# Kernel tuning notes

Hardware: AMD Instinct MI355X
Metric: run time of the kernel (lower is better)

Reference implementation:

```python
import jax, jax.numpy as jnp
import numpy as np

N_VIEWS = 8


def _trilinear(vol, pts):
    """Trilinear interpolation of vol [Nx,Ny,Nz] at pts [...,3] (voxel coords), zero outside."""
    nx, ny, nz = vol.shape
    x, y, z = pts[..., 0], pts[..., 1], pts[..., 2]
    x0f, y0f, z0f = jnp.floor(x), jnp.floor(y), jnp.floor(z)
    fx, fy, fz = x - x0f, y - y0f, z - z0f
    x0 = x0f.astype(jnp.int32)
    y0 = y0f.astype(jnp.int32)
    z0 = z0f.astype(jnp.int32)
    out = jnp.zeros(x.shape, vol.dtype)
    for dx in (0, 1):
        wx = fx if dx else (1.0 - fx)
        ix = x0 + dx
        vx = (ix >= 0) & (ix < nx)
        ixc = jnp.clip(ix, 0, nx - 1)
        for dy in (0, 1):
            wy = fy if dy else (1.0 - fy)
            iy = y0 + dy
            vxy = vx & (iy >= 0) & (iy < ny)
            iyc = jnp.clip(iy, 0, ny - 1)
            for dz in (0, 1):
                wz = fz if dz else (1.0 - fz)
                iz = z0 + dz
                valid = vxy & (iz >= 0) & (iz < nz)
                izc = jnp.clip(iz, 0, nz - 1)
                v = vol[ixc, iyc, izc]  # irregular gather
                out = out + jnp.where(valid, v, jnp.zeros((), vol.dtype)) * (wx * wy * wz)
    return out


def cone_project(vol, src_pos, det_center, det_u_vec, det_v_vec,
                 det_u, det_v, du, dv, voxel_spacing, n_steps):
    """Cone-beam forward projection: ray-march src->detector pixel, trilinear sampling."""
    nx, ny, nz = vol.shape
    us = (jnp.arange(det_u, dtype=vol.dtype) - (det_u - 1) / 2.0) * du
    vs = (jnp.arange(det_v, dtype=vol.dtype) - (det_v - 1) / 2.0) * dv
    # detector pixel world positions: [V, U, W, 3]
    det_pts = (det_center[:, None, None, :]
               + us[None, :, None, None] * det_u_vec[:, None, None, :]
               + vs[None, None, :, None] * det_v_vec[:, None, None, :])
    src = src_pos[:, None, None, :]            # [V,1,1,3]
    diff = det_pts - src                        # [V,U,W,3]
    ray_len = jnp.sqrt(jnp.sum(diff * diff, axis=-1))  # [V,U,W]
    step_len = ray_len / n_steps
    center = (jnp.array([nx, ny, nz], dtype=vol.dtype) - 1.0) / 2.0
    fracs = (jnp.arange(n_steps, dtype=vol.dtype) + 0.5) / n_steps

    def body(acc, s):
        p = src + s * diff                      # world coords [V,U,W,3]
        vox = p / voxel_spacing + center        # voxel coords
        return acc + _trilinear(vol, vox), None

    acc, _ = jax.lax.scan(body, jnp.zeros(ray_len.shape, vol.dtype), fracs)
    return acc * step_len


def setup_inputs() -> dict:
    key = jax.random.key(0)
    k1, k2 = jax.random.split(key)
    vol_shape = (256, 256, 256)
    x = 0.1 * jax.random.normal(k1, vol_shape, dtype=jnp.float32)
    reco = 0.1 * jax.random.normal(k2, vol_shape, dtype=jnp.float32)
    # circular cone-beam trajectory (units = voxels, spacing 1.0)
    sad, sdd = 400.0, 800.0  # source-axis / source-detector distance
    angles = np.linspace(0.0, np.pi, N_VIEWS, endpoint=False)
    ca, sa = np.cos(angles), np.sin(angles)
    zeros = np.zeros(N_VIEWS)
    src_pos = np.stack([-sad * ca, -sad * sa, zeros], axis=-1)
    det_center = np.stack([(sdd - sad) * ca, (sdd - sad) * sa, zeros], axis=-1)
    det_u_vec = np.stack([-sa, ca, zeros], axis=-1)
    det_v_vec = np.tile(np.array([0.0, 0.0, 1.0]), (N_VIEWS, 1))
    return {
        "x": x,
        "reco": reco,
        "src_pos": jnp.asarray(src_pos, jnp.float32),
        "det_center": jnp.asarray(det_center, jnp.float32),
        "det_u_vec": jnp.asarray(det_u_vec, jnp.float32),
        "det_v_vec": jnp.asarray(det_v_vec, jnp.float32),
        "du": 3.0,
        "dv": 3.0,
        "voxel_spacing": 1.0,
        "det_u": 128,
        "det_v": 128,
        "n_steps": 192,
    }


def reference(x, reco, src_pos, det_center, det_u_vec, det_v_vec,
              du, dv, voxel_spacing, det_u, det_v, n_steps):
    updated = x + reco
    sino = cone_project(updated, src_pos, det_center, det_u_vec, det_v_vec,
                        det_u, det_v, du, dv, voxel_spacing, n_steps)
    return sino, jax.nn.relu(updated)
```

## Files before the change

kernel.cpp:

```cpp
#include <hip/hip_runtime.h>
#include <math.h>

__global__ __launch_bounds__(256) void add_relu_kernel(
    const float* __restrict__ x,
    const float* __restrict__ reco,
    float* __restrict__ relu_out,
    float* __restrict__ upd_out,
    int n4)
{
    int i = blockIdx.x * blockDim.x + threadIdx.x;
    int stride = gridDim.x * blockDim.x;
    const float4* x4 = (const float4*)x;
    const float4* r4 = (const float4*)reco;
    float4* ro4 = (float4*)relu_out;
    float4* uo4 = (float4*)upd_out;
    for (; i < n4; i += stride) {
        float4 a = x4[i];
        float4 b = r4[i];
        float4 u;
        u.x = a.x + b.x;
        u.y = a.y + b.y;
        u.z = a.z + b.z;
        u.w = a.w + b.w;
        if (uo4) uo4[i] = u;
        float4 r;
        r.x = fmaxf(u.x, 0.0f);
        r.y = fmaxf(u.y, 0.0f);
        r.z = fmaxf(u.z, 0.0f);
        r.w = fmaxf(u.w, 0.0f);
        ro4[i] = r;
    }
}

template <int TWO>
__device__ __forceinline__ float fetch_corner(
    const float* __restrict__ vol_a,
    const float* __restrict__ vol_b,
    int ix, int iy, int iz,
    int nx, int ny, int nz)
{
    bool valid = (ix >= 0) & (ix < nx) & (iy >= 0) & (iy < ny) &
                 (iz >= 0) & (iz < nz);
    if (!valid) return 0.0f;
    int idx = (ix * ny + iy) * nz + iz;
    float v = vol_a[idx];
    if (TWO) v += vol_b[idx];
    return v;
}

__device__ __forceinline__ void clip_axis(float a, float b, float lo, float hi,
                                          float& t_lo, float& t_hi)
{
    if (fabsf(b) > 1e-6f) {
        float t0 = (lo - a) / b;
        float t1 = (hi - a) / b;
        float tmn = fminf(t0, t1);
        float tmx = fmaxf(t0, t1);
        t_lo = fmaxf(t_lo, tmn);
        t_hi = fminf(t_hi, tmx);
    } else {
        if (a <= lo || a >= hi) { t_lo = 1.0f; t_hi = 0.0f; }
    }
}

template <int TWO>
__global__ __launch_bounds__(256) void cone_project_seg_kernel(
    const float* __restrict__ vol_a,
    const float* __restrict__ vol_b,
    const float* __restrict__ src_pos,
    const float* __restrict__ det_center,
    const float* __restrict__ det_u_vec,
    const float* __restrict__ det_v_vec,
    const float* __restrict__ du_p,
    const float* __restrict__ dv_p,
    const float* __restrict__ spacing_p,
    const int* __restrict__ det_u_p,
    const int* __restrict__ det_v_p,
    const int* __restrict__ nsteps_p,
    float* __restrict__ sino,
    int n_views, int nx, int ny, int nz)
{
    const int det_u = *det_u_p;
    const int det_v = *det_v_p;
    const int n_steps = *nsteps_p;
    const float du = *du_p;
    const float dv = *dv_p;
    const float inv_sp = 1.0f / *spacing_p;

    const long total = (long)n_views * det_u * det_v;
    const int pix = threadIdx.x & 63;
    const int seg = threadIdx.x >> 6;
    const long idx = (long)blockIdx.x * 64 + pix;
    const bool live = idx < total;

    const long cidx = live ? idx : 0;
    const int v = (int)(cidx % det_v);
    const int u = (int)((cidx / det_v) % det_u);
    const int view = (int)(cidx / ((long)det_u * det_v));

    const float us = ((float)u - (det_u - 1) * 0.5f) * du;
    const float vs = ((float)v - (det_v - 1) * 0.5f) * dv;

    const float sx = src_pos[view * 3 + 0];
    const float sy = src_pos[view * 3 + 1];
    const float sz = src_pos[view * 3 + 2];

    const float dpx = det_center[view * 3 + 0] + us * det_u_vec[view * 3 + 0] + vs * det_v_vec[view * 3 + 0];
    const float dpy = det_center[view * 3 + 1] + us * det_u_vec[view * 3 + 1] + vs * det_v_vec[view * 3 + 1];
    const float dpz = det_center[view * 3 + 2] + us * det_u_vec[view * 3 + 2] + vs * det_v_vec[view * 3 + 2];

    const float dx = dpx - sx;
    const float dy = dpy - sy;
    const float dz = dpz - sz;
    const float ray_len = sqrtf(dx * dx + dy * dy + dz * dz);
    const float step_len = ray_len / (float)n_steps;

    const float cx = (nx - 1) * 0.5f;
    const float cy = (ny - 1) * 0.5f;
    const float cz = (nz - 1) * 0.5f;

    float t_lo = 0.0f, t_hi = 1.0f;
    clip_axis(sx * inv_sp + cx, dx * inv_sp, -1.0f, (float)nx, t_lo, t_hi);
    clip_axis(sy * inv_sp + cy, dy * inv_sp, -1.0f, (float)ny, t_lo, t_hi);
    clip_axis(sz * inv_sp + cz, dz * inv_sp, -1.0f, (float)nz, t_lo, t_hi);

    int i_min = 0, i_max = -1;
    if (t_hi > t_lo) {
        i_min = (int)floorf(t_lo * (float)n_steps - 0.5f) - 1;
        i_max = (int)ceilf(t_hi * (float)n_steps - 0.5f) + 1;
        i_min = max(i_min, 0);
        i_max = min(i_max, n_steps - 1);
    }
    if (!live) { i_min = 0; i_max = -1; }

    const int count = i_max - i_min + 1;
    const int per = (count + 3) >> 2;
    const int is = i_min + seg * per;
    const int ie = min(is + per - 1, i_max);

    const float inv_n = 1.0f / (float)n_steps;

    float acc = 0.0f;
    for (int i = is; i <= ie; ++i) {
        const float s = ((float)i + 0.5f) * inv_n;
        const float px = fmaf(s, dx, sx) * inv_sp + cx;
        const float py = fmaf(s, dy, sy) * inv_sp + cy;
        const float pz = fmaf(s, dz, sz) * inv_sp + cz;

        const float x0f = floorf(px);
        const float y0f = floorf(py);
        const float z0f = floorf(pz);
        const float fx = px - x0f;
        const float fy = py - y0f;
        const float fz = pz - z0f;
        const int x0 = (int)x0f;
        const int y0 = (int)y0f;
        const int z0 = (int)z0f;

        const float gx = 1.0f - fx;
        const float gy = 1.0f - fy;
        const float gz = 1.0f - fz;

        float samp = 0.0f;
        samp = fmaf(gx * gy * gz, fetch_corner<TWO>(vol_a, vol_b, x0,     y0,     z0,     nx, ny, nz), samp);
        samp = fmaf(gx * gy * fz, fetch_corner<TWO>(vol_a, vol_b, x0,     y0,     z0 + 1, nx, ny, nz), samp);
        samp = fmaf(gx * fy * gz, fetch_corner<TWO>(vol_a, vol_b, x0,     y0 + 1, z0,     nx, ny, nz), samp);
        samp = fmaf(gx * fy * fz, fetch_corner<TWO>(vol_a, vol_b, x0,     y0 + 1, z0 + 1, nx, ny, nz), samp);
        samp = fmaf(fx * gy * gz, fetch_corner<TWO>(vol_a, vol_b, x0 + 1, y0,     z0,     nx, ny, nz), samp);
        samp = fmaf(fx * gy * fz, fetch_corner<TWO>(vol_a, vol_b, x0 + 1, y0,     z0 + 1, nx, ny, nz), samp);
        samp = fmaf(fx * fy * gz, fetch_corner<TWO>(vol_a, vol_b, x0 + 1, y0 + 1, z0,     nx, ny, nz), samp);
        samp = fmaf(fx * fy * fz, fetch_corner<TWO>(vol_a, vol_b, x0 + 1, y0 + 1, z0 + 1, nx, ny, nz), samp);
        acc += samp;
    }

    __shared__ float red[256];
    red[threadIdx.x] = acc;
    __syncthreads();
    if (seg == 0 && live) {
        float tot = red[pix] + red[pix + 64] + red[pix + 128] + red[pix + 192];
        sino[idx] = tot * step_len;
    }
}

extern "C" void kernel_launch(void* const* d_in, const int* in_sizes, int n_in,
                              void* d_out, int out_size, void* d_ws, size_t ws_size,
                              hipStream_t stream) {
    const float* x          = (const float*)d_in[0];
    const float* reco       = (const float*)d_in[1];
    const float* src_pos    = (const float*)d_in[2];
    const float* det_center = (const float*)d_in[3];
    const float* det_u_vec  = (const float*)d_in[4];
    const float* det_v_vec  = (const float*)d_in[5];
    const float* du_p       = (const float*)d_in[6];
    const float* dv_p       = (const float*)d_in[7];
    const float* spacing_p  = (const float*)d_in[8];
    const int*   det_u_p    = (const int*)d_in[9];
    const int*   det_v_p    = (const int*)d_in[10];
    const int*   nsteps_p   = (const int*)d_in[11];

    const int n_vol = in_sizes[0];
    const int n_views = in_sizes[2] / 3;

    int n = 1;
    while ((long)(n + 1) * (n + 1) * (n + 1) <= (long)n_vol) ++n;
    const int nx = n, ny = n, nz = n;

    const int sino_size = out_size - n_vol;
    float* sino     = (float*)d_out;
    float* relu_out = (float*)d_out + sino_size;

    const bool use_ws = ws_size >= (size_t)n_vol * sizeof(float);
    float* upd = (float*)d_ws;

    const int n4 = n_vol / 4;
    add_relu_kernel<<<2048, 256, 0, stream>>>(
        x, reco, relu_out, use_ws ? upd : nullptr, n4);

    const int blocks = (sino_size + 63) / 64;
    if (use_ws) {
        cone_project_seg_kernel<0><<<blocks, 256, 0, stream>>>(
            upd, nullptr,
            src_pos, det_center, det_u_vec, det_v_vec,
            du_p, dv_p, spacing_p, det_u_p, det_v_p, nsteps_p,
            sino, n_views, nx, ny, nz);
    } else {
        cone_project_seg_kernel<1><<<blocks, 256, 0, stream>>>(
            x, reco,
            src_pos, det_center, det_u_vec, det_v_vec,
            du_p, dv_p, spacing_p, det_u_p, det_v_p, nsteps_p,
            sino, n_views, nx, ny, nz);
    }
}
```

Baseline: 238.1 us.

## Fuse add-relu and projection into one kernel with interleaved blocks

Merges the elementwise add+relu and the cone-beam projection into a single launch, spreading elementwise blocks evenly among projection blocks. The projector now reads x and reco directly and sums them per corner instead of reading a precomputed workspace volume. An interior fast path skips per-corner bounds checks. Each pixel's ray is split into eight segments instead of four. The trade is one launch and no workspace round-trip, paid for with twice the gather traffic per sample.

```diff
diff --git a/kernel.cpp b/kernel.cpp
--- a/kernel.cpp
+++ b/kernel.cpp
@@ -1,39 +1,10 @@
 #include <hip/hip_runtime.h>
 #include <math.h>
 
-__global__ __launch_bounds__(256) void add_relu_kernel(
-    const float* __restrict__ x,
-    const float* __restrict__ reco,
-    float* __restrict__ relu_out,
-    float* __restrict__ upd_out,
-    int n4)
-{
-    int i = blockIdx.x * blockDim.x + threadIdx.x;
-    int stride = gridDim.x * blockDim.x;
-    const float4* x4 = (const float4*)x;
-    const float4* r4 = (const float4*)reco;
-    float4* ro4 = (float4*)relu_out;
-    float4* uo4 = (float4*)upd_out;
-    for (; i < n4; i += stride) {
-        float4 a = x4[i];
-        float4 b = r4[i];
-        float4 u;
-        u.x = a.x + b.x;
-        u.y = a.y + b.y;
-        u.z = a.z + b.z;
-        u.w = a.w + b.w;
-        if (uo4) uo4[i] = u;
-        float4 r;
-        r.x = fmaxf(u.x, 0.0f);
-        r.y = fmaxf(u.y, 0.0f);
-        r.z = fmaxf(u.z, 0.0f);
-        r.w = fmaxf(u.w, 0.0f);
-        ro4[i] = r;
-    }
-}
-
-template <int TWO>
-__device__ __forceinline__ float fetch_corner(
+typedef float nfloat4 __attribute__((ext_vector_type(4)));
+
+
+__device__ __forceinline__ float fetch_corner2(
     const float* __restrict__ vol_a,
     const float* __restrict__ vol_b,
     int ix, int iy, int iz,
@@ -43,9 +14,7 @@
                  (iz >= 0) & (iz < nz);
     if (!valid) return 0.0f;
     int idx = (ix * ny + iy) * nz + iz;
-    float v = vol_a[idx];
-    if (TWO) v += vol_b[idx];
-    return v;
+    return vol_a[idx] + vol_b[idx];
 }
 
 __device__ __forceinline__ void clip_axis(float a, float b, float lo, float hi,
@@ -63,10 +32,9 @@
     }
 }
 
-template <int TWO>
-__global__ __launch_bounds__(256) void cone_project_seg_kernel(
-    const float* __restrict__ vol_a,
-    const float* __restrict__ vol_b,
+__global__ __launch_bounds__(256) void fused_kernel(
+    const float* __restrict__ x,
+    const float* __restrict__ reco,
     const float* __restrict__ src_pos,
     const float* __restrict__ det_center,
     const float* __restrict__ det_u_vec,
@@ -78,8 +46,37 @@
     const int* __restrict__ det_v_p,
     const int* __restrict__ nsteps_p,
     float* __restrict__ sino,
+    float* __restrict__ relu_out,
+    int n4,
+    int ew_blocks,
     int n_views, int nx, int ny, int nz)
 {
+    const int b = blockIdx.x;
+    const int total_b = gridDim.x;
+    const long ew_before = ((long)b * ew_blocks) / total_b;
+    const bool is_ew = (((long)(b + 1) * ew_blocks) / total_b) > ew_before;
+
+    if (is_ew) {
+        const int ew_id = (int)ew_before;
+        const nfloat4* x4 = (const nfloat4*)x;
+        const nfloat4* r4 = (const nfloat4*)reco;
+        nfloat4* ro4 = (nfloat4*)relu_out;
+        int i = ew_id * 256 + threadIdx.x;
+        const int stride = ew_blocks * 256;
+        for (; i < n4; i += stride) {
+            nfloat4 a = x4[i];
+            nfloat4 c = r4[i];
+            nfloat4 u = a + c;
+            nfloat4 r;
+            r.x = fmaxf(u.x, 0.f); r.y = fmaxf(u.y, 0.f);
+            r.z = fmaxf(u.z, 0.f); r.w = fmaxf(u.w, 0.f);
+            ro4[i] = r;
+        }
+        return;
+    }
+
+    const int pb = (int)(b - ew_before);
+
     const int det_u = *det_u_p;
     const int det_v = *det_v_p;
     const int n_steps = *nsteps_p;
@@ -88,9 +85,9 @@
     const float inv_sp = 1.0f / *spacing_p;
 
     const long total = (long)n_views * det_u * det_v;
-    const int pix = threadIdx.x & 63;
-    const int seg = threadIdx.x >> 6;
-    const long idx = (long)blockIdx.x * 64 + pix;
+    const int pix = threadIdx.x & 31;
+    const int seg = threadIdx.x >> 5;
+    const long idx = (long)pb * 32 + pix;
     const bool live = idx < total;
 
     const long cidx = live ? idx : 0;
@@ -134,7 +131,7 @@
     if (!live) { i_min = 0; i_max = -1; }
 
     const int count = i_max - i_min + 1;
-    const int per = (count + 3) >> 2;
+    const int per = (count + 7) >> 3;
     const int is = i_min + seg * per;
     const int ie = min(is + per - 1, i_max);
 
@@ -161,15 +158,41 @@
         const float gy = 1.0f - fy;
         const float gz = 1.0f - fz;
 
+        const bool interior = (x0 >= 0) & (x0 + 1 < nx) &
+                              (y0 >= 0) & (y0 + 1 < ny) &
+                              (z0 >= 0) & (z0 + 1 < nz);
+
         float samp = 0.0f;
-        samp = fmaf(gx * gy * gz, fetch_corner<TWO>(vol_a, vol_b, x0,     y0,     z0,     nx, ny, nz), samp);
-        samp = fmaf(gx * gy * fz, fetch_corner<TWO>(vol_a, vol_b, x0,     y0,     z0 + 1, nx, ny, nz), samp);
-        samp = fmaf(gx * fy * gz, fetch_corner<TWO>(vol_a, vol_b, x0,     y0 + 1, z0,     nx, ny, nz), samp);
-        samp = fmaf(gx * fy * fz, fetch_corner<TWO>(vol_a, vol_b, x0,     y0 + 1, z0 + 1, nx, ny, nz), samp);
-        samp = fmaf(fx * gy * gz, fetch_corner<TWO>(vol_a, vol_b, x0 + 1, y0,     z0,     nx, ny, nz), samp);
-        samp = fmaf(fx * gy * fz, fetch_corner<TWO>(vol_a, vol_b, x0 + 1, y0,     z0 + 1, nx, ny, nz), samp);
-        samp = fmaf(fx * fy * gz, fetch_corner<TWO>(vol_a, vol_b, x0 + 1, y0 + 1, z0,     nx, ny, nz), samp);
-        samp = fmaf(fx * fy * fz, fetch_corner<TWO>(vol_a, vol_b, x0 + 1, y0 + 1, z0 + 1, nx, ny, nz), samp);
+        if (interior) {
+            const int base = (x0 * ny + y0) * nz + z0;
+            const float* pa = x + base;
+            const float* pc = reco + base;
+            const float v000 = pa[0]            + pc[0];
+            const float v001 = pa[1]            + pc[1];
+            const float v010 = pa[nz]           + pc[nz];
+            const float v011 = pa[nz + 1]       + pc[nz + 1];
+            const float v100 = pa[ny * nz]      + pc[ny * nz];
+            const float v101 = pa[ny * nz + 1]  + pc[ny * nz + 1];
+            const float v110 = pa[ny * nz + nz] + pc[ny * nz + nz];
+            const float v111 = pa[ny * nz + nz + 1] + pc[ny * nz + nz + 1];
+            samp = fmaf(gx * gy * gz, v000, samp);
+            samp = fmaf(gx * gy * fz, v001, samp);
+            samp = fmaf(gx * fy * gz, v010, samp);
+            samp = fmaf(gx * fy * fz, v011, samp);
+            samp = fmaf(fx * gy * gz, v100, samp);
+            samp = fmaf(fx * gy * fz, v101, samp);
+            samp = fmaf(fx * fy * gz, v110, samp);
+            samp = fmaf(fx * fy * fz, v111, samp);
+        } else {
+            samp = fmaf(gx * gy * gz, fetch_corner2(x, reco, x0,     y0,     z0,     nx, ny, nz), samp);
+            samp = fmaf(gx * gy * fz, fetch_corner2(x, reco, x0,     y0,     z0 + 1, nx, ny, nz), samp);
+            samp = fmaf(gx * fy * gz, fetch_corner2(x, reco, x0,     y0 + 1, z0,     nx, ny, nz), samp);
+            samp = fmaf(gx * fy * fz, fetch_corner2(x, reco, x0,     y0 + 1, z0 + 1, nx, ny, nz), samp);
+            samp = fmaf(fx * gy * gz, fetch_corner2(x, reco, x0 + 1, y0,     z0,     nx, ny, nz), samp);
+            samp = fmaf(fx * gy * fz, fetch_corner2(x, reco, x0 + 1, y0,     z0 + 1, nx, ny, nz), samp);
+            samp = fmaf(fx * fy * gz, fetch_corner2(x, reco, x0 + 1, y0 + 1, z0,     nx, ny, nz), samp);
+            samp = fmaf(fx * fy * fz, fetch_corner2(x, reco, x0 + 1, y0 + 1, z0 + 1, nx, ny, nz), samp);
+        }
         acc += samp;
     }
 
@@ -177,7 +200,8 @@
     red[threadIdx.x] = acc;
     __syncthreads();
     if (seg == 0 && live) {
-        float tot = red[pix] + red[pix + 64] + red[pix + 128] + red[pix + 192];
+        float tot = red[pix]       + red[pix + 32]  + red[pix + 64]  + red[pix + 96] +
+                    red[pix + 128] + red[pix + 160] + red[pix + 192] + red[pix + 224];
         sino[idx] = tot * step_len;
     }
 }
@@ -209,25 +233,15 @@
     float* sino     = (float*)d_out;
     float* relu_out = (float*)d_out + sino_size;
 
-    const bool use_ws = ws_size >= (size_t)n_vol * sizeof(float);
-    float* upd = (float*)d_ws;
-
     const int n4 = n_vol / 4;
-    add_relu_kernel<<<2048, 256, 0, stream>>>(
-        x, reco, relu_out, use_ws ? upd : nullptr, n4);
-
-    const int blocks = (sino_size + 63) / 64;
-    if (use_ws) {
-        cone_project_seg_kernel<0><<<blocks, 256, 0, stream>>>(
-            upd, nullptr,
-            src_pos, det_center, det_u_vec, det_v_vec,
-            du_p, dv_p, spacing_p, det_u_p, det_v_p, nsteps_p,
-            sino, n_views, nx, ny, nz);
-    } else {
-        cone_project_seg_kernel<1><<<blocks, 256, 0, stream>>>(
-            x, reco,
-            src_pos, det_center, det_u_vec, det_v_vec,
-            du_p, dv_p, spacing_p, det_u_p, det_v_p, nsteps_p,
-            sino, n_views, nx, ny, nz);
-    }
-}
+    const int ew_blocks   = 2048;
+    const int proj_blocks = (sino_size + 31) / 32;
+    const int total_blocks = ew_blocks + proj_blocks;
+
+    fused_kernel<<<total_blocks, 256, 0, stream>>>(
+        x, reco,
+        src_pos, det_center, det_u_vec, det_v_vec,
+        du_p, dv_p, spacing_p, det_u_p, det_v_p, nsteps_p,
+        sino, relu_out,
+        n4, ew_blocks, n_views, nx, ny, nz);
+}
```

Result: slower. 253.7 us (+6.5%).
